# Optimization experiments

Measured on AMD Instinct MI355X. Metric: run time of the kernel, lower is better.

The kernel has to match this reference:

```python
import jax, jax.numpy as jnp
import numpy as np

IN_DIM = 128
HID = 128
OUT_DIM = 16
DICT_LEN = 400000
N_GATES = 4


def setup_inputs() -> dict:
    key = jax.random.key(0)
    ks = jax.random.split(key, 13)
    s = 0.05  # small init scale (stand-in for orthogonal init)
    return {
        "x_t": jax.random.normal(ks[0], (1, 1, IN_DIM), jnp.float32),
        "h": jax.random.normal(ks[1], (1, 1, HID), jnp.float32) * 0.1,
        "c": jax.random.normal(ks[2], (1, 1, HID), jnp.float32) * 0.1,
        "W_i2h": jax.random.normal(ks[3], ((N_GATES + 1) * HID, IN_DIM), jnp.float32) * s,
        "b_i2h": jnp.zeros(((N_GATES + 1) * HID,), jnp.float32),
        "W_h2h": jax.random.normal(ks[4], ((N_GATES + 1) * HID, HID), jnp.float32) * s,
        "b_h2h": jnp.zeros(((N_GATES + 1) * HID,), jnp.float32),
        "mem_keys": jax.random.normal(ks[5], (DICT_LEN, IN_DIM), jnp.float32),
        "mem_vals": jax.random.normal(ks[6], (DICT_LEN, HID), jnp.float32),
        "W_actor": jax.random.normal(ks[7], (OUT_DIM, HID), jnp.float32) * s,
        "b_actor": jnp.zeros((OUT_DIM,), jnp.float32),
        "W_critic": jax.random.normal(ks[8], (1, HID), jnp.float32) * s,
        "b_critic": jnp.zeros((1,), jnp.float32),
    }


def reference(x_t, h, c, W_i2h, b_i2h, W_h2h, b_h2h, mem_keys, mem_vals,
              W_actor, b_actor, W_critic, b_critic):
    # flatten [1, B, D] -> [B, D] (B == 1)
    x = x_t.reshape(x_t.shape[1], -1)
    hh = h.reshape(h.shape[1], -1)
    cc = c.reshape(c.shape[1], -1)
    hd = hh.shape[-1]

    # fused gate preactivation: i2h(x) + h2h(h), shape [1, 5*H]
    preact = x @ W_i2h.T + b_i2h + hh @ W_h2h.T + b_h2h
    gates = jax.nn.sigmoid(preact[:, :N_GATES * hd])
    f_t = gates[:, :hd]
    i_t = gates[:, hd:2 * hd]
    o_t = gates[:, 2 * hd:3 * hd]
    r_t = gates[:, 3 * hd:4 * hd]
    c_new = jnp.tanh(preact[:, N_GATES * hd:])
    c_t = f_t * cc + i_t * c_new

    # DND read: l2-kernel similarity over all stored keys, softmax-weighted value sum
    d2 = jnp.sum((mem_keys - x) ** 2, axis=-1)          # [L]
    sim = -jnp.sqrt(d2 + 1e-6)                           # F.pairwise_distance eps
    w = jax.nn.softmax(sim)                              # [L]
    m_t = jnp.tanh(w @ mem_vals)[None, :]                # [1, H]

    c_t = c_t + r_t * m_t
    h_t = o_t * jnp.tanh(c_t)

    # A2C heads
    pi = jax.nn.softmax(h_t @ W_actor.T + b_actor, axis=-1)  # [1, OUT]
    v = h_t @ W_critic.T + b_critic                          # [1, 1]

    # DND write: append (key=x_t, val=c_t), drop oldest (fixed-capacity dict)
    keys_new = jnp.concatenate([x, mem_keys[:-1]], axis=0)
    vals_new = jnp.concatenate([c_t, mem_vals[:-1]], axis=0)

    out = jnp.concatenate([pi.ravel(), v.ravel(), h_t.ravel(), c_t.ravel()])
    return out, keys_new, vals_new
```

## Files before the change

### kernel.cpp

```cpp
#include <hip/hip_runtime.h>
#include <hip/hip_bf16.h>
#include <math.h>

#define DICT 400000
#define D 128
#define NPAIR (DICT / 2)
#define G1 2048
#define KEYS_OFF 273
#define VALS_OFF (273 + DICT * D)
#define SHIFT 16.0f

typedef float vfloat4 __attribute__((ext_vector_type(4)));

__global__ __launch_bounds__(256) void k_pre(const float* __restrict__ Wi,
                                             const float* __restrict__ bi,
                                             const float* __restrict__ Wh,
                                             const float* __restrict__ bh,
                                             const float* __restrict__ x,
                                             const float* __restrict__ h,
                                             float* __restrict__ pre) {
    const int lane = threadIdx.x & 63;
    const int row = blockIdx.x * 4 + (threadIdx.x >> 6);
    if (row >= 640) return;
    float2 xv = reinterpret_cast<const float2*>(x)[lane];
    float2 hv = reinterpret_cast<const float2*>(h)[lane];
    float2 wi = reinterpret_cast<const float2*>(Wi + row * D)[lane];
    float2 wh = reinterpret_cast<const float2*>(Wh + row * D)[lane];
    float dot = wi.x * xv.x + wi.y * xv.y + wh.x * hv.x + wh.y * hv.y;
#pragma unroll
    for (int off = 32; off; off >>= 1) dot += __shfl_xor(dot, off);
    if (lane == 0) pre[row] = dot + bi[row] + bh[row];
}

__global__ __launch_bounds__(256) void k_dict(const float* __restrict__ keys,
                                              const float* __restrict__ vals,
                                              const float* __restrict__ x,
                                              float* __restrict__ keys_new,
                                              float* __restrict__ vals_new,
                                              float* __restrict__ partials) {
    const int tid = threadIdx.x;
    const int lane = tid & 63;
    const int half = lane >> 5;
    const int hl = lane & 31;
    const int wv = tid >> 6;
    const int sl = (lane & 32) + ((hl + 1) & 31);
    const float4 xv = reinterpret_cast<const float4*>(x)[hl];

    const int R = (NPAIR + G1 - 1) / G1;
    const int base = blockIdx.x * R;
    const int iend = min(R, NPAIR - base);

    vfloat4 acc = (vfloat4)(0.f);
    float den = 0.f;

    for (int i = wv; i < iend; i += 4) {
        const int p = base + i;
        const int row = 2 * p + half;
        vfloat4 kv = __builtin_nontemporal_load(
            reinterpret_cast<const vfloat4*>(keys + (size_t)row * D) + hl);
        vfloat4 vv = __builtin_nontemporal_load(
            reinterpret_cast<const vfloat4*>(vals + (size_t)row * D) + hl);

        if (row < DICT - 1) {
            float* kdst = keys_new + (size_t)(row + 1) * D;
            float* vdst = vals_new + (size_t)(row + 1) * D;
            float knx = __shfl(kv.x, sl), kny = __shfl(kv.y, sl), knz = __shfl(kv.z, sl);
            float vnx = __shfl(vv.x, sl), vny = __shfl(vv.y, sl), vnz = __shfl(vv.z, sl);
            if (hl < 31) {
                vfloat4 ks; ks.x = kv.w; ks.y = knx; ks.z = kny; ks.w = knz;
                vfloat4 vs; vs.x = vv.w; vs.y = vnx; vs.z = vny; vs.w = vnz;
                reinterpret_cast<vfloat4*>(kdst + 3)[hl] = ks;
                reinterpret_cast<vfloat4*>(vdst + 3)[hl] = vs;
            }
            if (hl == 0) {
                kdst[0] = kv.x; kdst[1] = kv.y; kdst[2] = kv.z;
                vdst[0] = vv.x; vdst[1] = vv.y; vdst[2] = vv.z;
            }
            if (hl == 31) {
                kdst[127] = kv.w;
                vdst[127] = vv.w;
            }
        }

        float dx = kv.x - xv.x, dy = kv.y - xv.y, dz = kv.z - xv.z, dw = kv.w - xv.w;
        float d2 = dx * dx + dy * dy + dz * dz + dw * dw;
#pragma unroll
        for (int off = 16; off; off >>= 1) d2 += __shfl_xor(d2, off);
        float e = __expf(SHIFT - sqrtf(d2 + 1e-6f));
        acc.x += e * vv.x; acc.y += e * vv.y;
        acc.z += e * vv.z; acc.w += e * vv.w;
        den += e;
    }

    acc.x += __shfl_xor(acc.x, 32);
    acc.y += __shfl_xor(acc.y, 32);
    acc.z += __shfl_xor(acc.z, 32);
    acc.w += __shfl_xor(acc.w, 32);
    den += __shfl_xor(den, 32);

    __shared__ float lnum[4][128];
    __shared__ float lden[4];
    if (lane < 32) {
        lnum[wv][hl * 4 + 0] = acc.x;
        lnum[wv][hl * 4 + 1] = acc.y;
        lnum[wv][hl * 4 + 2] = acc.z;
        lnum[wv][hl * 4 + 3] = acc.w;
    }
    if (lane == 0) lden[wv] = den;
    __syncthreads();
    if (tid < 128) {
        float s = lnum[0][tid] + lnum[1][tid] + lnum[2][tid] + lnum[3][tid];
        partials[(size_t)tid * G1 + blockIdx.x] = s;
    } else if (tid == 128) {
        partials[(size_t)128 * G1 + blockIdx.x] = lden[0] + lden[1] + lden[2] + lden[3];
    }
}

__global__ __launch_bounds__(256) void k_red(const float* __restrict__ partials,
                                             float* __restrict__ red) {
    const int j = blockIdx.x;
    float s = 0.f;
    for (int b = threadIdx.x; b < G1; b += 256) s += partials[(size_t)j * G1 + b];
#pragma unroll
    for (int off = 32; off; off >>= 1) s += __shfl_xor(s, off);
    __shared__ float w4[4];
    if ((threadIdx.x & 63) == 0) w4[threadIdx.x >> 6] = s;
    __syncthreads();
    if (threadIdx.x == 0) red[j] = w4[0] + w4[1] + w4[2] + w4[3];
}

__global__ __launch_bounds__(256) void k_tail(const float* __restrict__ red,
                                              const float* __restrict__ pre,
                                              const float* __restrict__ x,
                                              const float* __restrict__ c,
                                              const float* __restrict__ Wa,
                                              const float* __restrict__ ba,
                                              const float* __restrict__ Wc,
                                              const float* __restrict__ bc,
                                              float* __restrict__ out) {
    __shared__ float sh_h[128];
    __shared__ float sh_logit[16];
    const int tid = threadIdx.x;
    if (tid < 128) {
        float den = red[128];
        float m = tanhf(red[tid] / den);
        float f  = 1.f / (1.f + __expf(-pre[tid]));
        float i_ = 1.f / (1.f + __expf(-pre[128 + tid]));
        float o  = 1.f / (1.f + __expf(-pre[256 + tid]));
        float r  = 1.f / (1.f + __expf(-pre[384 + tid]));
        float cn = tanhf(pre[512 + tid]);
        float ct = f * c[tid] + i_ * cn + r * m;
        float ht = o * tanhf(ct);
        sh_h[tid] = ht;
        out[17 + tid] = ht;
        out[145 + tid] = ct;
        out[KEYS_OFF + tid] = x[tid];
        out[VALS_OFF + tid] = ct;
    }
    __syncthreads();
    if (tid < 16) {
        float l = ba[tid];
        for (int j = 0; j < 128; ++j) l += Wa[tid * D + j] * sh_h[j];
        sh_logit[tid] = l;
    } else if (tid == 16) {
        float v = bc[0];
        for (int j = 0; j < 128; ++j) v += Wc[j] * sh_h[j];
        out[16] = v;
    }
    __syncthreads();
    if (tid == 0) {
        float mx = sh_logit[0];
        for (int k = 1; k < 16; ++k) mx = fmaxf(mx, sh_logit[k]);
        float e[16];
        float s = 0.f;
        for (int k = 0; k < 16; ++k) { e[k] = __expf(sh_logit[k] - mx); s += e[k]; }
        for (int k = 0; k < 16; ++k) out[k] = e[k] / s;
    }
}

extern "C" void kernel_launch(void* const* d_in, const int* in_sizes, int n_in,
                              void* d_out, int out_size, void* d_ws, size_t ws_size,
                              hipStream_t stream) {
    const float* x    = (const float*)d_in[0];
    const float* h    = (const float*)d_in[1];
    const float* c    = (const float*)d_in[2];
    const float* Wi   = (const float*)d_in[3];
    const float* bi   = (const float*)d_in[4];
    const float* Wh   = (const float*)d_in[5];
    const float* bh   = (const float*)d_in[6];
    const float* keys = (const float*)d_in[7];
    const float* vals = (const float*)d_in[8];
    const float* Wa   = (const float*)d_in[9];
    const float* ba   = (const float*)d_in[10];
    const float* Wc   = (const float*)d_in[11];
    const float* bc   = (const float*)d_in[12];
    float* out = (float*)d_out;

    char* ws = (char*)d_ws;
    float* red      = (float*)(ws + 0);
    float* pre      = (float*)(ws + 1024);
    float* partials = (float*)(ws + 4096);

    k_pre<<<160, 256, 0, stream>>>(Wi, bi, Wh, bh, x, h, pre);
    k_dict<<<G1, 256, 0, stream>>>(keys, vals, x, out + KEYS_OFF, out + VALS_OFF, partials);
    k_red<<<129, 256, 0, stream>>>(partials, red);
    k_tail<<<1, 256, 0, stream>>>(red, pre, x, c, Wa, ba, Wc, bc, out);
}
```

Baseline: 210.3 us.

## Give each wave a contiguous row range and emit 16B-aligned shifted dictionary stores

Each wave now processes a contiguous run of row pairs instead of striding by four, so the one-row-shifted output it writes is also contiguous. The old scheme wrote rows at a 3-float offset, which meant misaligned vector stores plus scalar edge stores on every row. The new path carries the previous iteration's registers and shuffles them across the wave so that each lane writes an aligned vfloat4, with separate head and tail fixups per wave segment. The final block keeps the old path, and the new logic adds register pressure and more complex boundary handling.

```diff
diff --git a/kernel.cpp b/kernel.cpp
--- a/kernel.cpp
+++ b/kernel.cpp
@@ -44,52 +44,111 @@
     const int hl = lane & 31;
     const int wv = tid >> 6;
     const int sl = (lane & 32) + ((hl + 1) & 31);
+    const int idx3 = (lane + 3) & 63;
+    const int idx4 = (lane + 4) & 63;
     const float4 xv = reinterpret_cast<const float4*>(x)[hl];
 
     const int R = (NPAIR + G1 - 1) / G1;
     const int base = blockIdx.x * R;
-    const int iend = min(R, NPAIR - base);
+    const int iend = max(0, min(R, NPAIR - base));
+    const bool legacy = (base + iend == NPAIR);
+
+    const int q = iend >> 2, r = iend & 3;
+    const int p0 = base + wv * q + min(wv, r);
+    const int np = q + (wv < r ? 1 : 0);
+    const size_t W0 = (size_t)(2 * p0 + 1) * 128;
 
     vfloat4 acc = (vfloat4)(0.f);
     float den = 0.f;
-
-    for (int i = wv; i < iend; i += 4) {
-        const int p = base + i;
+    vfloat4 pk = (vfloat4)(0.f), pv = (vfloat4)(0.f);
+
+    for (int i = 0; i < np; ++i) {
+        const int p = p0 + i;
         const int row = 2 * p + half;
         vfloat4 kv = __builtin_nontemporal_load(
             reinterpret_cast<const vfloat4*>(keys + (size_t)row * D) + hl);
         vfloat4 vv = __builtin_nontemporal_load(
             reinterpret_cast<const vfloat4*>(vals + (size_t)row * D) + hl);
 
-        if (row < DICT - 1) {
-            float* kdst = keys_new + (size_t)(row + 1) * D;
-            float* vdst = vals_new + (size_t)(row + 1) * D;
-            float knx = __shfl(kv.x, sl), kny = __shfl(kv.y, sl), knz = __shfl(kv.z, sl);
-            float vnx = __shfl(vv.x, sl), vny = __shfl(vv.y, sl), vnz = __shfl(vv.z, sl);
-            if (hl < 31) {
-                vfloat4 ks; ks.x = kv.w; ks.y = knx; ks.z = kny; ks.w = knz;
-                vfloat4 vs; vs.x = vv.w; vs.y = vnx; vs.z = vny; vs.w = vnz;
-                reinterpret_cast<vfloat4*>(kdst + 3)[hl] = ks;
-                reinterpret_cast<vfloat4*>(vdst + 3)[hl] = vs;
+        {
+            float dx = kv.x - xv.x, dy = kv.y - xv.y, dz = kv.z - xv.z, dw = kv.w - xv.w;
+            float d2 = dx * dx + dy * dy + dz * dz + dw * dw;
+#pragma unroll
+            for (int off = 16; off; off >>= 1) d2 += __shfl_xor(d2, off);
+            float e = __expf(SHIFT - sqrtf(d2 + 1e-6f));
+            acc.x += e * vv.x; acc.y += e * vv.y;
+            acc.z += e * vv.z; acc.w += e * vv.w;
+            den += e;
+        }
+
+        if (legacy) {
+            if (row < DICT - 1) {
+                float* kdst = keys_new + (size_t)(row + 1) * D;
+                float* vdst = vals_new + (size_t)(row + 1) * D;
+                float knx = __shfl(kv.x, sl), kny = __shfl(kv.y, sl), knz = __shfl(kv.z, sl);
+                float vnx = __shfl(vv.x, sl), vny = __shfl(vv.y, sl), vnz = __shfl(vv.z, sl);
+                if (hl < 31) {
+                    vfloat4 ks; ks.x = kv.w; ks.y = knx; ks.z = kny; ks.w = knz;
+                    vfloat4 vs; vs.x = vv.w; vs.y = vnx; vs.z = vny; vs.w = vnz;
+                    reinterpret_cast<vfloat4*>(kdst + 3)[hl] = ks;
+                    reinterpret_cast<vfloat4*>(vdst + 3)[hl] = vs;
+                }
+                if (hl == 0) {
+                    kdst[0] = kv.x; kdst[1] = kv.y; kdst[2] = kv.z;
+                    vdst[0] = vv.x; vdst[1] = vv.y; vdst[2] = vv.z;
+                }
+                if (hl == 31) { kdst[127] = kv.w; vdst[127] = vv.w; }
             }
-            if (hl == 0) {
-                kdst[0] = kv.x; kdst[1] = kv.y; kdst[2] = kv.z;
-                vdst[0] = vv.x; vdst[1] = vv.y; vdst[2] = vv.z;
+        } else {
+            if (i == 0) {
+                if (lane < 4) {
+                    float* kd = keys_new + W0 + 4 * lane;
+                    float* vd = vals_new + W0 + 4 * lane;
+                    int f = 4 * lane;
+                    if (f + 0 < 15) { kd[0] = kv.x; vd[0] = vv.x; }
+                    if (f + 1 < 15) { kd[1] = kv.y; vd[1] = vv.y; }
+                    if (f + 2 < 15) { kd[2] = kv.z; vd[2] = vv.z; }
+                    if (f + 3 < 15) { kd[3] = kv.w; vd[3] = vv.w; }
+                }
+            } else {
+                vfloat4 ks, vs;
+                float s;
+                s = (lane < 3) ? kv.w : pk.w;  ks.x = __shfl(s, idx3);
+                s = (lane < 4) ? kv.x : pk.x;  ks.y = __shfl(s, idx4);
+                s = (lane < 4) ? kv.y : pk.y;  ks.z = __shfl(s, idx4);
+                s = (lane < 4) ? kv.z : pk.z;  ks.w = __shfl(s, idx4);
+                s = (lane < 3) ? vv.w : pv.w;  vs.x = __shfl(s, idx3);
+                s = (lane < 4) ? vv.x : pv.x;  vs.y = __shfl(s, idx4);
+                s = (lane < 4) ? vv.y : pv.y;  vs.z = __shfl(s, idx4);
+                s = (lane < 4) ? vv.z : pv.z;  vs.w = __shfl(s, idx4);
+                size_t off = W0 + 15 + 256 * (size_t)(i - 1) + 4 * lane;
+                *reinterpret_cast<vfloat4*>(keys_new + off) = ks;
+                *reinterpret_cast<vfloat4*>(vals_new + off) = vs;
             }
-            if (hl == 31) {
-                kdst[127] = kv.w;
-                vdst[127] = vv.w;
-            }
-        }
-
-        float dx = kv.x - xv.x, dy = kv.y - xv.y, dz = kv.z - xv.z, dw = kv.w - xv.w;
-        float d2 = dx * dx + dy * dy + dz * dz + dw * dw;
-#pragma unroll
-        for (int off = 16; off; off >>= 1) d2 += __shfl_xor(d2, off);
-        float e = __expf(SHIFT - sqrtf(d2 + 1e-6f));
-        acc.x += e * vv.x; acc.y += e * vv.y;
-        acc.z += e * vv.z; acc.w += e * vv.w;
-        den += e;
+        }
+        pk = kv; pv = vv;
+    }
+
+    if (!legacy && np > 0) {
+        const int j = np - 1;
+        vfloat4 ks, vs;
+        ks.x = __shfl(pk.w, idx3);
+        ks.y = __shfl(pk.x, idx4);
+        ks.z = __shfl(pk.y, idx4);
+        ks.w = __shfl(pk.z, idx4);
+        vs.x = __shfl(pv.w, idx3);
+        vs.y = __shfl(pv.x, idx4);
+        vs.z = __shfl(pv.y, idx4);
+        vs.w = __shfl(pv.z, idx4);
+        if (lane < 60) {
+            size_t off = W0 + 15 + 256 * (size_t)j + 4 * lane;
+            *reinterpret_cast<vfloat4*>(keys_new + off) = ks;
+            *reinterpret_cast<vfloat4*>(vals_new + off) = vs;
+        }
+        if (lane == 63) {
+            keys_new[W0 + 256 * (size_t)np - 1] = pk.w;
+            vals_new[W0 + 256 * (size_t)np - 1] = pv.w;
+        }
     }
 
     acc.x += __shfl_xor(acc.x, 32);
@@ -109,8 +168,8 @@
     if (lane == 0) lden[wv] = den;
     __syncthreads();
     if (tid < 128) {
-        float s = lnum[0][tid] + lnum[1][tid] + lnum[2][tid] + lnum[3][tid];
-        partials[(size_t)tid * G1 + blockIdx.x] = s;
+        float ssum = lnum[0][tid] + lnum[1][tid] + lnum[2][tid] + lnum[3][tid];
+        partials[(size_t)tid * G1 + blockIdx.x] = ssum;
     } else if (tid == 128) {
         partials[(size_t)128 * G1 + blockIdx.x] = lden[0] + lden[1] + lden[2] + lden[3];
     }
```

Measured after the change: 210.7 us. No clear change (+0.2%).
